# Kernel tuning notes

Measured on AMD Instinct MI355X. Metric: run time of the kernel, lower is better.

The kernel has to match this reference:

```python
import jax, jax.numpy as jnp
import numpy as np

D_MODEL = 1024

def setup_inputs() -> dict:
    key = jax.random.key(0)
    ks = jax.random.split(key, 7)
    x = jax.random.normal(ks[0], (4, 2048, D_MODEL), dtype=jnp.float32)
    s = 1.0 / np.sqrt(D_MODEL)
    Wq = jax.random.uniform(ks[1], (D_MODEL, D_MODEL), jnp.float32, -s, s)
    bq = jax.random.uniform(ks[2], (D_MODEL,), jnp.float32, -s, s)
    Wk = jax.random.uniform(ks[3], (D_MODEL, D_MODEL), jnp.float32, -s, s)
    bk = jax.random.uniform(ks[4], (D_MODEL,), jnp.float32, -s, s)
    Wv = jax.random.uniform(ks[5], (D_MODEL, D_MODEL), jnp.float32, -s, s)
    bv = jax.random.uniform(ks[6], (D_MODEL,), jnp.float32, -s, s)
    return {"x": x, "Wq": Wq, "bq": bq, "Wk": Wk, "bk": bk, "Wv": Wv, "bv": bv}

def reference(x, Wq, bq, Wk, bk, Wv, bv):
    # single-head self-attention: q,k,v are [B, S, D]
    q = x @ Wq + bq
    k = x @ Wk + bk
    v = x @ Wv + bv
    scale = 1.0 / jnp.sqrt(jnp.asarray(D_MODEL, x.dtype))
    scores = jnp.einsum('bsd,btd->bst', q, k) * scale  # [B, S, S]
    attn = jax.nn.softmax(scores, axis=-1)
    return jnp.einsum('bst,btd->bsd', attn, v)
```

## Files before the change

### kernel.cpp

```cpp
#include <hip/hip_runtime.h>
#include <hip/hip_bf16.h>
#include <stdint.h>


typedef __attribute__((ext_vector_type(8))) short short8;
typedef __attribute__((ext_vector_type(4))) float f32x4;

__device__ __forceinline__ unsigned short f2bf(float f) {
  union { float f; uint32_t u; } c; c.f = f;
  uint32_t u = c.u;
  u += 0x7FFFu + ((u >> 16) & 1u);
  return (unsigned short)(u >> 16);
}

__device__ __forceinline__ void gl16(const void* g, void* l) {
  __builtin_amdgcn_global_load_lds(
      (const __attribute__((address_space(1))) unsigned int*)g,
      (__attribute__((address_space(3))) unsigned int*)l, 16, 0, 0);
}

template <int EPI>
__device__ __forceinline__ void gemm_body(
    const short* __restrict__ A, int lda, long sAz,
    const short* __restrict__ B, int ldb, long sBz,
    void* __restrict__ Cv, int ldc, long sCz,
    int K, float scale,
    const float* __restrict__ bias0, const float* __restrict__ bias1,
    const float* __restrict__ bias2, float* __restrict__ rowsum)
{
  __shared__ short lds[18432];

  const int tid  = threadIdx.x;
  const int lane = tid & 63;
  const int wid  = tid >> 6;
  const int z    = blockIdx.z;
  const long tileM = (long)blockIdx.y * 128;
  const long tileN = (long)blockIdx.x * 128;
  const short* Az = A + (long)z * sAz;
  const short* Bz = B + (long)z * sBz;

  const int c0 = tid, c1 = 256 + tid;
  const short* gA0 = Az + (tileM + (c0 >> 2)) * lda + (c0 & 3) * 8;
  const short* gA1 = Az + (tileM + (c1 >> 2)) * lda + (c1 & 3) * 8;
  const short* gB0 = Bz + (tileN + (c0 >> 2)) * ldb + (c0 & 3) * 8;
  const short* gB1 = Bz + (tileN + (c1 >> 2)) * ldb + (c1 & 3) * 8;

  const int fr = lane & 15, quad = lane >> 4;
  const int waveM = (wid >> 1) * 64, waveN = (wid & 1) * 64;

  f32x4 acc[4][4] = {};

  const int T = K >> 5;

  {
    short* base = lds;
    gl16(gA0, base + c0 * 8);
    gl16(gA1, base + c1 * 8);
    gl16(gB0, base + 4096 + c0 * 8);
    gl16(gB1, base + 4096 + c1 * 8);
  }

  for (int t = 0; t < T; ++t) {
    __syncthreads();
    if (t + 1 < T) {
      const int kt = (t + 1) << 5;
      short* base = lds + ((t + 1) & 1) * 8192;
      gl16(gA0 + kt, base + c0 * 8);
      gl16(gA1 + kt, base + c1 * 8);
      gl16(gB0 + kt, base + 4096 + c0 * 8);
      gl16(gB1 + kt, base + 4096 + c1 * 8);
    }
    const short* sA = lds + (t & 1) * 8192;
    const short* sB = sA + 4096;
    short8 af[4], bf[4];
#pragma unroll
    for (int i = 0; i < 4; ++i)
      af[i] = *(const short8*)&sA[(waveM + i * 16 + fr) * 32 + quad * 8];
#pragma unroll
    for (int j = 0; j < 4; ++j)
      bf[j] = *(const short8*)&sB[(waveN + j * 16 + fr) * 32 + quad * 8];
#pragma unroll
    for (int i = 0; i < 4; ++i)
#pragma unroll
      for (int j = 0; j < 4; ++j)
        acc[i][j] = __builtin_amdgcn_mfma_f32_16x16x32_bf16(af[i], bf[j],
                                                            acc[i][j], 0, 0, 0);
  }

  if (EPI == 1) {
#pragma unroll
    for (int i = 0; i < 4; ++i)
#pragma unroll
      for (int j = 0; j < 4; ++j)
#pragma unroll
        for (int r = 0; r < 4; ++r)
          acc[i][j][r] = exp2f(acc[i][j][r] * scale);
#pragma unroll
    for (int i = 0; i < 4; ++i)
#pragma unroll
      for (int r = 0; r < 4; ++r) {
        float s = acc[i][0][r] + acc[i][1][r] + acc[i][2][r] + acc[i][3][r];
        s += __shfl_xor(s, 1);
        s += __shfl_xor(s, 2);
        s += __shfl_xor(s, 4);
        s += __shfl_xor(s, 8);
        if (fr == 0)
          atomicAdd(&rowsum[(long)z * 2048 + tileM + waveM + i * 16 + quad * 4 + r], s);
      }
  }

  if (EPI <= 1) {
    __syncthreads();
    short* scr = lds + wid * 4608;
    short* C = (short*)Cv + (long)z * sCz;
    const float* bias = (z == 0) ? bias0 : ((z == 1) ? bias1 : bias2);
#pragma unroll
    for (int j = 0; j < 4; ++j) {
      const float bv = (EPI == 0) ? bias[tileN + waveN + j * 16 + fr] : 0.0f;
#pragma unroll
      for (int i = 0; i < 4; ++i)
#pragma unroll
        for (int r = 0; r < 4; ++r)
          scr[(i * 16 + quad * 4 + r) * 72 + j * 16 + fr] =
              (short)f2bf(acc[i][j][r] + bv);
    }
#pragma unroll
    for (int c = 0; c < 8; ++c) {
      const int row = c * 8 + (lane >> 3);
      const int col = (lane & 7) * 8;
      short8 v = *(const short8*)&scr[row * 72 + col];
      *(short8*)(C + (tileM + waveM + row) * ldc + tileN + waveN + col) = v;
    }
  } else {
    float* C = (float*)Cv + (long)z * sCz;
#pragma unroll
    for (int i = 0; i < 4; ++i)
#pragma unroll
      for (int r = 0; r < 4; ++r) {
        const long gr = tileM + waveM + i * 16 + quad * 4 + r;
        const float rinv = 1.0f / rowsum[(long)z * 2048 + gr];
#pragma unroll
        for (int j = 0; j < 4; ++j)
          C[gr * ldc + tileN + waveN + j * 16 + fr] = acc[i][j][r] * rinv;
      }
  }
}

__global__ __launch_bounds__(256) void gemm_qkv(
    const short* A, int lda, long sAz, const short* B, int ldb, long sBz,
    void* Cv, int ldc, long sCz, int K, float scale,
    const float* b0, const float* b1, const float* b2, float* rs) {
  gemm_body<0>(A, lda, sAz, B, ldb, sBz, Cv, ldc, sCz, K, scale, b0, b1, b2, rs);
}
__global__ __launch_bounds__(256) void gemm_score(
    const short* A, int lda, long sAz, const short* B, int ldb, long sBz,
    void* Cv, int ldc, long sCz, int K, float scale,
    const float* b0, const float* b1, const float* b2, float* rs) {
  gemm_body<1>(A, lda, sAz, B, ldb, sBz, Cv, ldc, sCz, K, scale, b0, b1, b2, rs);
}
__global__ __launch_bounds__(256) void gemm_pv(
    const short* A, int lda, long sAz, const short* B, int ldb, long sBz,
    void* Cv, int ldc, long sCz, int K, float scale,
    const float* b0, const float* b1, const float* b2, float* rs) {
  gemm_body<2>(A, lda, sAz, B, ldb, sBz, Cv, ldc, sCz, K, scale, b0, b1, b2, rs);
}

__global__ __launch_bounds__(256) void prep(
    const float4* __restrict__ x, ushort4* __restrict__ xb,
    const float* __restrict__ Wq, const float* __restrict__ Wk,
    const float* __restrict__ Wv, short* __restrict__ WT,
    float* __restrict__ rs)
{
  __shared__ short tile[32][33];
  const int b = blockIdx.x;
  if (b < 8192) {
    const long i = (long)b * 256 + threadIdx.x;
    float4 v = x[i];
    ushort4 o;
    o.x = f2bf(v.x); o.y = f2bf(v.y); o.z = f2bf(v.z); o.w = f2bf(v.w);
    xb[i] = o;
  } else if (b < 11264) {
    const int idx = b - 8192;
    const int z = idx >> 10, rem = idx & 1023;
    const float* W = (z == 0) ? Wq : ((z == 1) ? Wk : Wv);
    short* d = WT + (long)z * 1024 * 1024;
    const int n0 = (rem & 31) * 32, d0 = (rem >> 5) * 32;
    const int tx = threadIdx.x & 31, ty = threadIdx.x >> 5;
#pragma unroll
    for (int p = 0; p < 4; ++p)
      tile[ty + p * 8][tx] = (short)f2bf(W[(long)(d0 + ty + p * 8) * 1024 + n0 + tx]);
    __syncthreads();
#pragma unroll
    for (int p = 0; p < 4; ++p)
      d[(long)(n0 + ty + p * 8) * 1024 + d0 + tx] = tile[tx][ty + p * 8];
  } else {
#pragma unroll
    for (int p = 0; p < 32; ++p)
      rs[p * 256 + threadIdx.x] = 0.0f;
  }
}

__global__ __launch_bounds__(256) void transpose_bf16(
    const short* __restrict__ src, short* __restrict__ dst)
{
  __shared__ short tile[32][33];
  const int z = blockIdx.z;
  const int d0 = blockIdx.x * 32, t0 = blockIdx.y * 32;
  const int tx = threadIdx.x & 31, ty = threadIdx.x >> 5;
  const short* s = src + (long)z * 2048 * 1024;
  short* d = dst + (long)z * 1024 * 2048;
#pragma unroll
  for (int p = 0; p < 4; ++p)
    tile[ty + p * 8][tx] = s[(long)(t0 + ty + p * 8) * 1024 + d0 + tx];
  __syncthreads();
#pragma unroll
  for (int p = 0; p < 4; ++p)
    d[(long)(d0 + ty + p * 8) * 2048 + t0 + tx] = tile[tx][ty + p * 8];
}

extern "C" void kernel_launch(void* const* d_in, const int* in_sizes, int n_in,
                              void* d_out, int out_size, void* d_ws, size_t ws_size,
                              hipStream_t stream) {
  const float* x  = (const float*)d_in[0];
  const float* Wq = (const float*)d_in[1];
  const float* bq = (const float*)d_in[2];
  const float* Wk = (const float*)d_in[3];
  const float* bk = (const float*)d_in[4];
  const float* Wv = (const float*)d_in[5];
  const float* bv = (const float*)d_in[6];

  char* ws = (char*)d_ws;
  short* xb  = (short*)(ws);
  short* wt  = (short*)(ws + 16777216);
  short* qkv = (short*)(ws + 23068672);
  short* Pp  = (short*)(ws + 73400320);
  float* rs  = (float*)(ws + 106954752);
  short* vT  = xb;

  prep<<<11265, 256, 0, stream>>>((const float4*)x, (ushort4*)xb,
                                  Wq, Wk, Wv, wt, rs);
  gemm_qkv<<<dim3(8, 64, 3), 256, 0, stream>>>(
      xb, 1024, 0L, wt, 1024, 1048576L, qkv, 1024, 8388608L,
      1024, 1.0f, bq, bk, bv, nullptr);
  transpose_bf16<<<dim3(32, 64, 4), 256, 0, stream>>>(qkv + 2L * 8388608, vT);
  gemm_score<<<dim3(16, 16, 4), 256, 0, stream>>>(
      qkv, 1024, 2097152L, qkv + 8388608, 1024, 2097152L, Pp, 2048, 4194304L,
      1024, 0.03125f * 1.44269504088896f, nullptr, nullptr, nullptr, rs);
  gemm_pv<<<dim3(8, 16, 4), 256, 0, stream>>>(
      Pp, 2048, 4194304L, vT, 2048, 2097152L, d_out, 1024, 2097152L,
      2048, 1.0f, nullptr, nullptr, nullptr, rs);
}
```

Measured before the change: 275.0 us.

## Fuse V transpose into QKV epilogue and remap tiles for XCD locality

Removes the separate bf16 transpose kernel by writing V directly in transposed layout from the QKV GEMM epilogue via the LDS scratch. Replaces 3D grids with a 1D grid whose block index is decoded so neighbouring tiles land on the same XCD, aiming to improve L2 reuse. Strides and trip counts become compile-time constants per mode. The transposed LDS writes may add bank conflicts in that epilogue.

Measured after the change: 265.8 us. -3.3%, faster.

```diff
diff --git a/kernel.cpp b/kernel.cpp
--- a/kernel.cpp
+++ b/kernel.cpp
@@ -19,38 +19,66 @@
       (__attribute__((address_space(3))) unsigned int*)l, 16, 0, 0);
 }
 
-template <int EPI>
-__device__ __forceinline__ void gemm_body(
-    const short* __restrict__ A, int lda, long sAz,
-    const short* __restrict__ B, int ldb, long sBz,
-    void* __restrict__ Cv, int ldc, long sCz,
-    int K, float scale,
+template <int MODE>
+__global__ __launch_bounds__(256) void gemm(
+    const short* __restrict__ A, const short* __restrict__ B,
+    void* __restrict__ Cv, short* __restrict__ vT, float scale,
     const float* __restrict__ bias0, const float* __restrict__ bias1,
     const float* __restrict__ bias2, float* __restrict__ rowsum)
 {
+  constexpr int  LDA = (MODE == 2) ? 2048 : 1024;
+  constexpr int  LDB = (MODE == 2) ? 2048 : 1024;
+  constexpr int  LDC = (MODE == 0) ? 1024 : ((MODE == 1) ? 2048 : 1024);
+  constexpr long SAZ = (MODE == 0) ? 0L : ((MODE == 1) ? 2097152L : 4194304L);
+  constexpr long SBZ = (MODE == 0) ? 1048576L : 2097152L;
+  constexpr long SCZ = (MODE == 0) ? 8388608L : ((MODE == 1) ? 4194304L : 2097152L);
+  constexpr int  T   = (MODE == 2) ? 64 : 32;
+
+  int z, tm, tn;
+  {
+    const int b = blockIdx.x;
+    if (MODE == 0) {
+      const int xcd = b & 7, r = b >> 3;
+      z = r >> 6;
+      const int mem = r & 63;
+      tm = xcd * 8 + (mem >> 3);
+      tn = mem & 7;
+    } else if (MODE == 1) {
+      const int xcd = b & 7, r = b >> 3;
+      z = r >> 5;
+      const int pair = (r >> 4) & 1, mem = r & 15;
+      const int s = pair * 8 + xcd;
+      tm = (s >> 2) * 4 + (mem >> 2);
+      tn = (s & 3) * 4 + (mem & 3);
+    } else {
+      const int s = b & 7, r = b >> 3;
+      z = r >> 4;
+      const int mem = r & 15;
+      tm = (s >> 1) * 4 + (mem >> 2);
+      tn = (s & 1) * 4 + (mem & 3);
+    }
+  }
+
   __shared__ short lds[18432];
 
   const int tid  = threadIdx.x;
   const int lane = tid & 63;
   const int wid  = tid >> 6;
-  const int z    = blockIdx.z;
-  const long tileM = (long)blockIdx.y * 128;
-  const long tileN = (long)blockIdx.x * 128;
-  const short* Az = A + (long)z * sAz;
-  const short* Bz = B + (long)z * sBz;
+  const long tileM = (long)tm * 128;
+  const long tileN = (long)tn * 128;
+  const short* Az = A + (long)z * SAZ;
+  const short* Bz = B + (long)z * SBZ;
 
   const int c0 = tid, c1 = 256 + tid;
-  const short* gA0 = Az + (tileM + (c0 >> 2)) * lda + (c0 & 3) * 8;
-  const short* gA1 = Az + (tileM + (c1 >> 2)) * lda + (c1 & 3) * 8;
-  const short* gB0 = Bz + (tileN + (c0 >> 2)) * ldb + (c0 & 3) * 8;
-  const short* gB1 = Bz + (tileN + (c1 >> 2)) * ldb + (c1 & 3) * 8;
+  const short* gA0 = Az + (tileM + (c0 >> 2)) * LDA + (c0 & 3) * 8;
+  const short* gA1 = Az + (tileM + (c1 >> 2)) * LDA + (c1 & 3) * 8;
+  const short* gB0 = Bz + (tileN + (c0 >> 2)) * LDB + (c0 & 3) * 8;
+  const short* gB1 = Bz + (tileN + (c1 >> 2)) * LDB + (c1 & 3) * 8;
 
   const int fr = lane & 15, quad = lane >> 4;
   const int waveM = (wid >> 1) * 64, waveN = (wid & 1) * 64;
 
   f32x4 acc[4][4] = {};
-
-  const int T = K >> 5;
 
   {
     short* base = lds;
@@ -87,7 +115,7 @@
                                                             acc[i][j], 0, 0, 0);
   }
 
-  if (EPI == 1) {
+  if (MODE == 1) {
 #pragma unroll
     for (int i = 0; i < 4; ++i)
 #pragma unroll
@@ -109,14 +137,37 @@
       }
   }
 
-  if (EPI <= 1) {
+  if (MODE == 0 && z == 2) {
     __syncthreads();
     short* scr = lds + wid * 4608;
-    short* C = (short*)Cv + (long)z * sCz;
-    const float* bias = (z == 0) ? bias0 : ((z == 1) ? bias1 : bias2);
 #pragma unroll
     for (int j = 0; j < 4; ++j) {
-      const float bv = (EPI == 0) ? bias[tileN + waveN + j * 16 + fr] : 0.0f;
+      const float bv = bias2[tileN + waveN + j * 16 + fr];
+#pragma unroll
+      for (int i = 0; i < 4; ++i)
+#pragma unroll
+        for (int r = 0; r < 4; ++r)
+          scr[(j * 16 + fr) * 72 + i * 16 + quad * 4 + r] =
+              (short)f2bf(acc[i][j][r] + bv);
+    }
+    const int gb = tm >> 4;
+    const long t0 = (long)(tm & 15) * 128 + waveM;
+#pragma unroll
+    for (int c = 0; c < 8; ++c) {
+      const int rr = c * 8 + (lane >> 3);
+      const int cc = (lane & 7) * 8;
+      short8 v = *(const short8*)&scr[rr * 72 + cc];
+      const long gd = tileN + waveN + rr;
+      *(short8*)(vT + ((long)gb << 21) + gd * 2048 + t0 + cc) = v;
+    }
+  } else if (MODE <= 1) {
+    __syncthreads();
+    short* scr = lds + wid * 4608;
+    short* C = (short*)Cv + (long)z * SCZ;
+    const float* bias = (z == 0) ? bias0 : bias1;
+#pragma unroll
+    for (int j = 0; j < 4; ++j) {
+      const float bv = (MODE == 0) ? bias[tileN + waveN + j * 16 + fr] : 0.0f;
 #pragma unroll
       for (int i = 0; i < 4; ++i)
 #pragma unroll
@@ -129,10 +180,10 @@
       const int row = c * 8 + (lane >> 3);
       const int col = (lane & 7) * 8;
       short8 v = *(const short8*)&scr[row * 72 + col];
-      *(short8*)(C + (tileM + waveM + row) * ldc + tileN + waveN + col) = v;
+      *(short8*)(C + (tileM + waveM + row) * LDC + tileN + waveN + col) = v;
     }
   } else {
-    float* C = (float*)Cv + (long)z * sCz;
+    float* C = (float*)Cv + (long)z * SCZ;
 #pragma unroll
     for (int i = 0; i < 4; ++i)
 #pragma unroll
@@ -141,28 +192,9 @@
         const float rinv = 1.0f / rowsum[(long)z * 2048 + gr];
 #pragma unroll
         for (int j = 0; j < 4; ++j)
-          C[gr * ldc + tileN + waveN + j * 16 + fr] = acc[i][j][r] * rinv;
+          C[gr * LDC + tileN + waveN + j * 16 + fr] = acc[i][j][r] * rinv;
       }
   }
-}
-
-__global__ __launch_bounds__(256) void gemm_qkv(
-    const short* A, int lda, long sAz, const short* B, int ldb, long sBz,
-    void* Cv, int ldc, long sCz, int K, float scale,
-    const float* b0, const float* b1, const float* b2, float* rs) {
-  gemm_body<0>(A, lda, sAz, B, ldb, sBz, Cv, ldc, sCz, K, scale, b0, b1, b2, rs);
-}
-__global__ __launch_bounds__(256) void gemm_score(
-    const short* A, int lda, long sAz, const short* B, int ldb, long sBz,
-    void* Cv, int ldc, long sCz, int K, float scale,
-    const float* b0, const float* b1, const float* b2, float* rs) {
-  gemm_body<1>(A, lda, sAz, B, ldb, sBz, Cv, ldc, sCz, K, scale, b0, b1, b2, rs);
-}
-__global__ __launch_bounds__(256) void gemm_pv(
-    const short* A, int lda, long sAz, const short* B, int ldb, long sBz,
-    void* Cv, int ldc, long sCz, int K, float scale,
-    const float* b0, const float* b1, const float* b2, float* rs) {
-  gemm_body<2>(A, lda, sAz, B, ldb, sBz, Cv, ldc, sCz, K, scale, b0, b1, b2, rs);
 }
 
 __global__ __launch_bounds__(256) void prep(
@@ -200,24 +232,6 @@
   }
 }
 
-__global__ __launch_bounds__(256) void transpose_bf16(
-    const short* __restrict__ src, short* __restrict__ dst)
-{
-  __shared__ short tile[32][33];
-  const int z = blockIdx.z;
-  const int d0 = blockIdx.x * 32, t0 = blockIdx.y * 32;
-  const int tx = threadIdx.x & 31, ty = threadIdx.x >> 5;
-  const short* s = src + (long)z * 2048 * 1024;
-  short* d = dst + (long)z * 1024 * 2048;
-#pragma unroll
-  for (int p = 0; p < 4; ++p)
-    tile[ty + p * 8][tx] = s[(long)(t0 + ty + p * 8) * 1024 + d0 + tx];
-  __syncthreads();
-#pragma unroll
-  for (int p = 0; p < 4; ++p)
-    d[(long)(d0 + ty + p * 8) * 2048 + t0 + tx] = tile[tx][ty + p * 8];
-}
-
 extern "C" void kernel_launch(void* const* d_in, const int* in_sizes, int n_in,
                               void* d_out, int out_size, void* d_ws, size_t ws_size,
                               hipStream_t stream) {
@@ -235,18 +249,14 @@
   short* qkv = (short*)(ws + 23068672);
   short* Pp  = (short*)(ws + 73400320);
   float* rs  = (float*)(ws + 106954752);
-  short* vT  = xb;
+  short* vT  = qkv + 2L * 8388608;
 
   prep<<<11265, 256, 0, stream>>>((const float4*)x, (ushort4*)xb,
                                   Wq, Wk, Wv, wt, rs);
-  gemm_qkv<<<dim3(8, 64, 3), 256, 0, stream>>>(
-      xb, 1024, 0L, wt, 1024, 1048576L, qkv, 1024, 8388608L,
-      1024, 1.0f, bq, bk, bv, nullptr);
-  transpose_bf16<<<dim3(32, 64, 4), 256, 0, stream>>>(qkv + 2L * 8388608, vT);
-  gemm_score<<<dim3(16, 16, 4), 256, 0, stream>>>(
-      qkv, 1024, 2097152L, qkv + 8388608, 1024, 2097152L, Pp, 2048, 4194304L,
-      1024, 0.03125f * 1.44269504088896f, nullptr, nullptr, nullptr, rs);
-  gemm_pv<<<dim3(8, 16, 4), 256, 0, stream>>>(
-      Pp, 2048, 4194304L, vT, 2048, 2097152L, d_out, 1024, 2097152L,
-      2048, 1.0f, nullptr, nullptr, nullptr, rs);
-}
+  gemm<0><<<1536, 256, 0, stream>>>(xb, wt, qkv, vT, 1.0f, bq, bk, bv, nullptr);
+  gemm<1><<<1024, 256, 0, stream>>>(qkv, qkv + 8388608, Pp, nullptr,
+                                    0.03125f * 1.44269504088896f,
+                                    nullptr, nullptr, nullptr, rs);
+  gemm<2><<<512, 256, 0, stream>>>(Pp, vT, d_out, nullptr, 1.0f,
+                                   nullptr, nullptr, nullptr, rs);
+}
```
